# Performance work log

Measured on AMD Instinct MI355X. Metric: run time of the kernel, lower is better.

The kernel has to match this reference:

```python
import jax, jax.numpy as jnp
import numpy as np

FREQ_BANDS = 10
LN_EPS = 1e-5


def nerf_positional_encoding(x, L=FREQ_BANDS):
    # x: (..., 3) -> (..., 3*2*L). Per-frequency [sin(2^i x), cos(2^i x)].
    freqs = 2.0 ** jnp.arange(L, dtype=x.dtype)            # (L,)
    xb = x[..., None, :] * freqs[:, None]                  # (..., L, 3)
    enc = jnp.concatenate([jnp.sin(xb), jnp.cos(xb)], -1)  # (..., L, 6)
    return enc.reshape(x.shape[:-1] + (L * 6,))


def farthest_point_sampling(xyz, npoint):
    # xyz: (B, N, 3) -> (B, npoint) int32. Deterministic start at index 0
    # (torch version uses a random start; start choice is arbitrary for FPS).
    B, N, _ = xyz.shape
    binds = jnp.arange(B)

    def step(carry, _):
        dist, far = carry
        c = xyz[binds, far]                                # (B, 3)
        d = jnp.sum((xyz - c[:, None, :]) ** 2, axis=-1)   # (B, N)
        dist = jnp.minimum(dist, d)
        nxt = jnp.argmax(dist, axis=-1).astype(jnp.int32)
        return (dist, nxt), far

    init = (jnp.full((B, N), 1e10, xyz.dtype), jnp.zeros((B,), jnp.int32))
    _, idx = jax.lax.scan(step, init, None, length=npoint)
    return jnp.swapaxes(idx, 0, 1)                         # (B, npoint)


def _layernorm(x, g, b):
    m = jnp.mean(x, axis=-1, keepdims=True)
    v = jnp.var(x, axis=-1, keepdims=True)
    return (x - m) * jax.lax.rsqrt(v + LN_EPS) * g + b


def setup_inputs() -> dict:
    key = jax.random.key(0)
    ks = jax.random.split(key, 8)
    B, N, C = 8, 16384, 64
    d_in = C + 3 * 2 * FREQ_BANDS                          # 124
    dims = [d_in, 128, 128, 256]

    def lin(k, din, dout):
        return jax.random.normal(k, (din, dout), jnp.float32) / np.sqrt(din)

    return {
        "xyz": jax.random.normal(ks[0], (B, N, 3), jnp.float32),
        "features": jax.random.normal(ks[1], (B, N, C), jnp.float32),
        "W1": lin(ks[2], dims[0], dims[1]), "b1": jnp.zeros((dims[1],), jnp.float32),
        "g1": jnp.ones((dims[1],), jnp.float32), "be1": jnp.zeros((dims[1],), jnp.float32),
        "W2": lin(ks[3], dims[1], dims[2]), "b2": jnp.zeros((dims[2],), jnp.float32),
        "g2": jnp.ones((dims[2],), jnp.float32), "be2": jnp.zeros((dims[2],), jnp.float32),
        "W3": lin(ks[4], dims[2], dims[3]), "b3": jnp.zeros((dims[3],), jnp.float32),
        "npoint": 2048,
        "nsample": 32,
    }


def reference(xyz, features, W1, b1, g1, be1, W2, b2, g2, be2, W3, b3, npoint, nsample):
    # FPS centroids
    fps_idx = farthest_point_sampling(xyz, npoint)                 # (B, S)
    new_xyz = jnp.take_along_axis(xyz, fps_idx[..., None], axis=1) # (B, S, 3)

    # KNN: squared distances preserve topk ordering of cdist
    d2 = jnp.sum((new_xyz[:, :, None, :] - xyz[:, None, :, :]) ** 2, axis=-1)  # (B,S,N)
    _, knn_idx = jax.lax.top_k(-d2, nsample)                        # (B, S, k)

    gather = jax.vmap(lambda pts, idx: pts[idx])                    # (N,D),(S,k)->(S,k,D)
    grouped_xyz = gather(xyz, knn_idx)                              # (B, S, k, 3)
    rel_pos = grouped_xyz - new_xyz[:, :, None, :]
    rel_enc = nerf_positional_encoding(rel_pos)                     # (B, S, k, 60)

    grouped_feat = gather(features, knn_idx)                        # (B, S, k, C)
    h = jnp.concatenate([grouped_feat, rel_enc], axis=-1)           # (B, S, k, C+60)

    h = jax.nn.relu(_layernorm(h @ W1 + b1, g1, be1))
    h = jax.nn.relu(_layernorm(h @ W2 + b2, g2, be2))
    h = h @ W3 + b3                                                 # (B, S, k, 256)
    new_features = jnp.max(h, axis=2)                               # (B, S, 256)
    return new_xyz, new_features
```

## Files before the change

### kernel.cpp

```cpp
#include <hip/hip_runtime.h>
#include <cstdint>
#include <cstddef>

#define BATCH   8
#define NPTS    16384
#define CFEAT   64
#define NPOINT  2048
#define NSAMPLE 32
#define DIN     124
#define D1      128
#define D2      128
#define D3      256
#define LN_EPS  1e-5f

#define NFPS      8
#define NBLOCKS   256
#define KNN_ITEMS 128
#define MLP_ITEMS 2048
#define TOT_ITEMS (KNN_ITEMS + MLP_ITEMS)

#define SB_BYTES   19872
#define SMEM_BYTES (8 * SB_BYTES)

#define CTL_QHEAD   0
#define CTL_PROG    1024
#define CTL_KCNT    4096
#define CTL_KFLAG   16384
#define CTL_BYTES   32768

#define PTS16(F) F(0) F(1) F(2) F(3) F(4) F(5) F(6) F(7) \
                 F(8) F(9) F(10) F(11) F(12) F(13) F(14) F(15)

__attribute__((amdgpu_waves_per_eu(4, 4)))
__global__ __launch_bounds__(1024) void fused_kernel(
    const float* __restrict__ xyz, const float* __restrict__ features,
    const float* __restrict__ W1, const float* __restrict__ b1,
    const float* __restrict__ g1, const float* __restrict__ be1,
    const float* __restrict__ W2, const float* __restrict__ b2,
    const float* __restrict__ g2, const float* __restrict__ be2,
    const float* __restrict__ W3, const float* __restrict__ b3,
    int* __restrict__ knn_idx, unsigned char* __restrict__ ctl,
    float* __restrict__ new_xyz, float* __restrict__ out)
{
  __shared__ __align__(16) unsigned char smem[SMEM_BYTES];
  __shared__ unsigned s_item;
  const int t = threadIdx.x;

  unsigned* qhead = (unsigned*)(ctl + CTL_QHEAD);
#define PROG_AT(b)  ((int*)(ctl + CTL_PROG + (b) * 256))
#define KCNT_AT(k)  ((unsigned*)(ctl + CTL_KCNT + (k) * 64))
#define KFLAG_AT(k) ((unsigned*)(ctl + CTL_KFLAG + (k) * 64))

  if (blockIdx.x < NFPS) {
    const int b = blockIdx.x;
    const float* X = xyz + (size_t)b * NPTS * 3;

    float4 (*s_mind4)[1024] = reinterpret_cast<float4(*)[1024]>(smem);
    float* wvv = (float*)(smem + 65536);
    unsigned long long* s_packed = (unsigned long long*)(smem + 65600);
    float* cbuf = (float*)(smem + 65616);

#define DECLP(i) float px##i, py##i, pz##i;
    PTS16(DECLP)
#undef DECLP
#define LOADP(i) { int j = t + (i << 10);  \
    px##i = X[3 * j + 0];                  \
    py##i = X[3 * j + 1];                  \
    pz##i = X[3 * j + 2]; }
    PTS16(LOADP)
#undef LOADP
    s_mind4[0][t] = make_float4(1e10f, 1e10f, 1e10f, 1e10f);
    s_mind4[1][t] = make_float4(1e10f, 1e10f, 1e10f, 1e10f);
    s_mind4[2][t] = make_float4(1e10f, 1e10f, 1e10f, 1e10f);
    s_mind4[3][t] = make_float4(1e10f, 1e10f, 1e10f, 1e10f);

    if (t == 0) { cbuf[0] = X[0]; cbuf[1] = X[1]; cbuf[2] = X[2]; *s_packed = 0ull; }
    __syncthreads();

    for (int s = 0; s < NPOINT; ++s) {
      const float cx = cbuf[0], cy = cbuf[1], cz = cbuf[2];
      if (t == 0) {
        float* o = new_xyz + ((size_t)b * NPOINT + s) * 3;
        o[0] = cx; o[1] = cy; o[2] = cz;
        *s_packed = 0ull;
        if (((s + 1) & 15) == 0) {
          __builtin_amdgcn_fence(__ATOMIC_RELEASE, "agent");
          __hip_atomic_store(PROG_AT(b), s + 1, __ATOMIC_RELAXED,
                             __HIP_MEMORY_SCOPE_AGENT);
        }
      }
      if (s == NPOINT - 1) break;

      asm volatile("" : "+v"(px0), "+v"(px1), "+v"(px2), "+v"(px3),
                        "+v"(px4), "+v"(px5), "+v"(px6), "+v"(px7),
                        "+v"(px8), "+v"(px9), "+v"(px10), "+v"(px11),
                        "+v"(px12), "+v"(px13), "+v"(px14), "+v"(px15));
      asm volatile("" : "+v"(py0), "+v"(py1), "+v"(py2), "+v"(py3),
                        "+v"(py4), "+v"(py5), "+v"(py6), "+v"(py7),
                        "+v"(py8), "+v"(py9), "+v"(py10), "+v"(py11),
                        "+v"(py12), "+v"(py13), "+v"(py14), "+v"(py15));
      asm volatile("" : "+v"(pz0), "+v"(pz1), "+v"(pz2), "+v"(pz3),
                        "+v"(pz4), "+v"(pz5), "+v"(pz6), "+v"(pz7),
                        "+v"(pz8), "+v"(pz9), "+v"(pz10), "+v"(pz11),
                        "+v"(pz12), "+v"(pz13), "+v"(pz14), "+v"(pz15));

      float mybest = -1.0f;
#define DIST(i) ({                                                       \
    float dx_ = __fsub_rn(px##i, cx);                                    \
    float dy_ = __fsub_rn(py##i, cy);                                    \
    float dz_ = __fsub_rn(pz##i, cz);                                    \
    __fadd_rn(__fadd_rn(__fmul_rn(dx_, dx_), __fmul_rn(dy_, dy_)),       \
              __fmul_rn(dz_, dz_)); })
#define PACKSTEP(p, i0, i1, i2, i3) {                                    \
    float4 dv = s_mind4[p][t];                                           \
    dv.x = fminf(dv.x, DIST(i0));                                        \
    dv.y = fminf(dv.y, DIST(i1));                                        \
    dv.z = fminf(dv.z, DIST(i2));                                        \
    dv.w = fminf(dv.w, DIST(i3));                                        \
    s_mind4[p][t] = dv;                                                  \
    mybest = fmaxf(mybest, fmaxf(fmaxf(dv.x, dv.y), fmaxf(dv.z, dv.w))); }
      PACKSTEP(0, 0, 1, 2, 3)
      PACKSTEP(1, 4, 5, 6, 7)
      PACKSTEP(2, 8, 9, 10, 11)
      PACKSTEP(3, 12, 13, 14, 15)
#undef PACKSTEP
#undef DIST

      float wmax = mybest;
#pragma unroll
      for (int off = 32; off >= 1; off >>= 1)
        wmax = fmaxf(wmax, __shfl_xor(wmax, off));
      if ((t & 63) == 0) wvv[t >> 6] = wmax;
      __syncthreads();

      float4 v0 = *(const float4*)&wvv[0];
      float4 v1 = *(const float4*)&wvv[4];
      float4 v2 = *(const float4*)&wvv[8];
      float4 v3 = *(const float4*)&wvv[12];
      float g = fmaxf(
          fmaxf(fmaxf(fmaxf(v0.x, v0.y), fmaxf(v0.z, v0.w)),
                fmaxf(fmaxf(v1.x, v1.y), fmaxf(v1.z, v1.w))),
          fmaxf(fmaxf(fmaxf(v2.x, v2.y), fmaxf(v2.z, v2.w)),
                fmaxf(fmaxf(v3.x, v3.y), fmaxf(v3.z, v3.w))));

      if (mybest == g) {
        int kk = 16;
#pragma unroll
        for (int p = 3; p >= 0; --p) {
          float4 dv = s_mind4[p][t];
          if (dv.w == g) kk = 4 * p + 3;
          if (dv.z == g) kk = 4 * p + 2;
          if (dv.y == g) kk = 4 * p + 1;
          if (dv.x == g) kk = 4 * p + 0;
        }
        unsigned idx = (unsigned)(t + (kk << 10));
        unsigned long long pk =
            ((unsigned long long)__float_as_uint(g) << 32) | (unsigned)(~idx);
        atomicMax(s_packed, pk);
      }
      __syncthreads();

      unsigned long long gp = *s_packed;
      int widx = (int)(~(unsigned)(gp & 0xffffffffull)) & 0x3fff;
      if (t == (widx & 1023)) {
        int c = widx >> 10;
#define OWNK(i) if (c == i) { cbuf[0] = px##i; cbuf[1] = py##i; cbuf[2] = pz##i; }
        PTS16(OWNK)
#undef OWNK
      }
      __syncthreads();
    }
    return;
  }

  for (;;) {
    __syncthreads();
    if (t == 0)
      s_item = __hip_atomic_fetch_add(qhead, 1u, __ATOMIC_RELAXED,
                                      __HIP_MEMORY_SCOPE_AGENT);
    __syncthreads();
    unsigned item = s_item;
    if (item >= TOT_ITEMS) return;

    if (item < KNN_ITEMS) {
      const int k = (int)item;
      const int b = k >> 4;
      const int chunk = k & 15;
      const int lane = t & 63;
      const int wid  = t >> 6;
      const int gidbase = b * NPOINT + chunk * 128 + wid * 8;
      const int need = chunk * 128 + wid * 8 + 8;
      const float* X = xyz + (size_t)b * NPTS * 3;

      if (lane == 0) {
        while (__hip_atomic_load(PROG_AT(b), __ATOMIC_RELAXED,
                                 __HIP_MEMORY_SCOPE_AGENT) < need)
          __builtin_amdgcn_s_sleep(64);
      }
      __builtin_amdgcn_fence(__ATOMIC_ACQUIRE, "agent");

      float cx[8], cy[8], cz[8];
#pragma unroll
      for (int c = 0; c < 8; ++c) {
        const float* p = new_xyz + (size_t)(gidbase + c) * 3;
        cx[c] = p[0]; cy[c] = p[1]; cz[c] = p[2];
      }
      float qd[8]; int qi[8]; float T[8];
#pragma unroll
      for (int c = 0; c < 8; ++c) { qd[c] = 3.4e38f; qi[c] = 0; T[c] = 3.4e38f; }

      for (int base = 0; base < NPTS; base += 64) {
        const int j = base + lane;
        const float x = X[3 * j + 0];
        const float y = X[3 * j + 1];
        const float z = X[3 * j + 2];
#pragma unroll
        for (int c = 0; c < 8; ++c) {
          float dx = __fsub_rn(x, cx[c]);
          float dy = __fsub_rn(y, cy[c]);
          float dz = __fsub_rn(z, cz[c]);
          float v  = __fadd_rn(__fadd_rn(__fmul_rn(dx, dx), __fmul_rn(dy, dy)),
                               __fmul_rn(dz, dz));
          unsigned long long m = __ballot(v < T[c]);
          while (m) {
            int bit = __ffsll(m) - 1;
            m &= m - 1;
            float vb = __shfl(v, bit);
            if (vb < T[c]) {
              int   jb = base + bit;
              float du = __shfl_up(qd[c], 1);
              int   iu = __shfl_up(qi[c], 1);
              bool c2 = (lane > 0) && (vb < du);
              bool c1 = vb < qd[c];
              qd[c] = c2 ? du : (c1 ? vb : qd[c]);
              qi[c] = c2 ? iu : (c1 ? jb : qi[c]);
              T[c] = __shfl(qd[c], 31);
            }
          }
        }
      }
#pragma unroll
      for (int c = 0; c < 8; ++c) {
        if (lane < 32) knn_idx[(size_t)(gidbase + c) * NSAMPLE + lane] = qi[c];
      }
      __builtin_amdgcn_fence(__ATOMIC_RELEASE, "agent");
      if (lane == 0) {
        unsigned d = __hip_atomic_fetch_add(KCNT_AT(k), 1u, __ATOMIC_ACQ_REL,
                                            __HIP_MEMORY_SCOPE_AGENT);
        if (d == 15u)
          __hip_atomic_store(KFLAG_AT(k), 1u, __ATOMIC_RELEASE,
                             __HIP_MEMORY_SCOPE_AGENT);
      }
    } else {
      const int m = (int)(item - KNN_ITEMS);
      const int gbase = m << 3;
      const int b = gbase / NPOINT;
      const int sb = t >> 7;
      const int t127 = t & 127;
      const int g = gbase + sb;

      if (t == 0) {
        while (__hip_atomic_load(KFLAG_AT(m >> 4), __ATOMIC_RELAXED,
                                 __HIP_MEMORY_SCOPE_AGENT) == 0u)
          __builtin_amdgcn_s_sleep(64);
      }
      __syncthreads();
      __builtin_amdgcn_fence(__ATOMIC_ACQUIRE, "agent");

      unsigned char* base_ = smem + sb * SB_BYTES;
      float* bufT = (float*)base_;
      float (*red)[4][2] = (float(*)[4][2])(base_ + 18432);
      float (*lnp)[2]    = (float(*)[2])(base_ + 19456);
      int*   ki          = (int*)(base_ + 19712);
      float* cen         = (float*)(base_ + 19840);

      if (t127 < 32) ki[t127] = knn_idx[(size_t)g * NSAMPLE + t127];
      if (t127 < 3)  cen[t127] = new_xyz[(size_t)g * 3 + t127];
      __syncthreads();

      {
        int r = t127 & 31, cs = (t127 >> 5) << 4;
        const float* frow = features + ((size_t)b * NPTS + ki[r]) * CFEAT + cs;
#pragma unroll
        for (int u = 0; u < 4; ++u) {
          float4 f = *(const float4*)(frow + 4 * u);
          bufT[(cs + 4 * u + 0) * 36 + r] = f.x;
          bufT[(cs + 4 * u + 1) * 36 + r] = f.y;
          bufT[(cs + 4 * u + 2) * 36 + r] = f.z;
          bufT[(cs + 4 * u + 3) * 36 + r] = f.w;
        }
      }
      if (t127 < 32) {
        const float* p = xyz + ((size_t)b * NPTS + ki[t127]) * 3;
        float rx = p[0] - cen[0];
        float ry = p[1] - cen[1];
        float rz = p[2] - cen[2];
#pragma unroll
        for (int l = 0; l < 10; ++l) {
          float sc = (float)(1 << l);
          float ax = rx * sc, ay = ry * sc, az = rz * sc;
          int bbi = (64 + l * 6) * 36 + t127;
          bufT[bbi + 0 * 36] = __sinf(ax);
          bufT[bbi + 1 * 36] = __sinf(ay);
          bufT[bbi + 2 * 36] = __sinf(az);
          bufT[bbi + 3 * 36] = __cosf(ax);
          bufT[bbi + 4 * 36] = __cosf(ay);
          bufT[bbi + 5 * 36] = __cosf(az);
        }
      }
      __syncthreads();

      float acc[32];
      {
        float bias = b1[t127];
#pragma unroll
        for (int r = 0; r < 32; ++r) acc[r] = bias;
        for (int i = 0; i < DIN; ++i) {
          float w = W1[i * D1 + t127];
          const float* hr = &bufT[i * 36];
#pragma unroll
          for (int r = 0; r < 32; ++r) acc[r] = fmaf(hr[r], w, acc[r]);
        }
      }
      {
        __syncthreads();
#pragma unroll
        for (int r = 0; r < 32; ++r) bufT[t127 * 36 + r] = acc[r];
        __syncthreads();
        {
          int r = t127 & 31, seg = t127 >> 5;
          float s = 0.f, ss = 0.f;
#pragma unroll
          for (int u = 0; u < 32; ++u) {
            float v = bufT[(seg * 32 + u) * 36 + r];
            s += v; ss = fmaf(v, v, ss);
          }
          red[r][seg][0] = s; red[r][seg][1] = ss;
        }
        __syncthreads();
        if (t127 < 32) {
          float s  = red[t127][0][0] + red[t127][1][0] + red[t127][2][0] + red[t127][3][0];
          float ss = red[t127][0][1] + red[t127][1][1] + red[t127][2][1] + red[t127][3][1];
          float mm = s * (1.0f / D1);
          float var = ss * (1.0f / D1) - mm * mm;
          lnp[t127][0] = mm;
          lnp[t127][1] = rsqrtf(var + LN_EPS);
        }
        __syncthreads();
        float gg = g1[t127], bb = be1[t127];
#pragma unroll
        for (int r = 0; r < 32; ++r) {
          float v = (acc[r] - lnp[r][0]) * lnp[r][1];
          v = fmaf(v, gg, bb);
          bufT[t127 * 36 + r] = fmaxf(v, 0.f);
        }
        __syncthreads();
      }
      {
        float bias = b2[t127];
#pragma unroll
        for (int r = 0; r < 32; ++r) acc[r] = bias;
        for (int i = 0; i < D1; ++i) {
          float w = W2[i * D2 + t127];
          const float* hr = &bufT[i * 36];
#pragma unroll
          for (int r = 0; r < 32; ++r) acc[r] = fmaf(hr[r], w, acc[r]);
        }
      }
      {
        __syncthreads();
#pragma unroll
        for (int r = 0; r < 32; ++r) bufT[t127 * 36 + r] = acc[r];
        __syncthreads();
        {
          int r = t127 & 31, seg = t127 >> 5;
          float s = 0.f, ss = 0.f;
#pragma unroll
          for (int u = 0; u < 32; ++u) {
            float v = bufT[(seg * 32 + u) * 36 + r];
            s += v; ss = fmaf(v, v, ss);
          }
          red[r][seg][0] = s; red[r][seg][1] = ss;
        }
        __syncthreads();
        if (t127 < 32) {
          float s  = red[t127][0][0] + red[t127][1][0] + red[t127][2][0] + red[t127][3][0];
          float ss = red[t127][0][1] + red[t127][1][1] + red[t127][2][1] + red[t127][3][1];
          float mm = s * (1.0f / D2);
          float var = ss * (1.0f / D2) - mm * mm;
          lnp[t127][0] = mm;
          lnp[t127][1] = rsqrtf(var + LN_EPS);
        }
        __syncthreads();
        float gg = g2[t127], bb = be2[t127];
#pragma unroll
        for (int r = 0; r < 32; ++r) {
          float v = (acc[r] - lnp[r][0]) * lnp[r][1];
          v = fmaf(v, gg, bb);
          bufT[t127 * 36 + r] = fmaxf(v, 0.f);
        }
        __syncthreads();
      }
      float* of = out + (size_t)g * D3;
#pragma unroll 1
      for (int half = 0; half < 2; ++half) {
        int col = t127 + (half << 7);
        float a[32];
        float bias = b3[col];
#pragma unroll
        for (int r = 0; r < 32; ++r) a[r] = bias;
        for (int i = 0; i < D2; ++i) {
          float w = W3[i * D3 + col];
          const float* hr = &bufT[i * 36];
#pragma unroll
          for (int r = 0; r < 32; ++r) a[r] = fmaf(hr[r], w, a[r]);
        }
        float m0 = a[0];
#pragma unroll
        for (int r = 1; r < 32; ++r) m0 = fmaxf(m0, a[r]);
        of[col] = m0;
      }
      __syncthreads();
    }
  }
#undef PROG_AT
#undef KCNT_AT
#undef KFLAG_AT
}

extern "C" void kernel_launch(void* const* d_in, const int* in_sizes, int n_in,
                              void* d_out, int out_size, void* d_ws, size_t ws_size,
                              hipStream_t stream) {
  const float* xyz      = (const float*)d_in[0];
  const float* features = (const float*)d_in[1];
  const float* W1  = (const float*)d_in[2];
  const float* b1  = (const float*)d_in[3];
  const float* g1  = (const float*)d_in[4];
  const float* be1 = (const float*)d_in[5];
  const float* W2  = (const float*)d_in[6];
  const float* b2  = (const float*)d_in[7];
  const float* g2  = (const float*)d_in[8];
  const float* be2 = (const float*)d_in[9];
  const float* W3  = (const float*)d_in[10];
  const float* b3  = (const float*)d_in[11];

  float* new_xyz  = (float*)d_out;
  float* new_feat = (float*)d_out + (size_t)BATCH * NPOINT * 3;

  int* knn_idx = (int*)d_ws;
  unsigned char* ctl = (unsigned char*)d_ws +
                       (size_t)BATCH * NPOINT * NSAMPLE * 4;

  hipMemsetAsync(ctl, 0, CTL_BYTES, stream);
  fused_kernel<<<dim3(NBLOCKS), dim3(1024), 0, stream>>>(
      xyz, features, W1, b1, g1, be1, W2, b2, g2, be2, W3, b3,
      knn_idx, ctl, new_xyz, new_feat);
}
```

Baseline: 5.087 ms.

## Spatially sort FPS points into Morton grid cells and skip waves by bounding-box bound

Before the FPS loop, each batch's points are bucketed into an 8x8x8 Morton-ordered grid through global scratch arrays and reloaded so every wavefront holds a spatially compact set. Each wave keeps its bounding box and skips the distance update when the box's lower-bound distance to the new centroid cannot beat the wave's current maximum min-distance. Ties in the argmax are broken by original index to keep the output identical. This adds a one-time sort with atomics and a global round trip, plus extra LDS and register pressure, in exchange for skipping most distance work in later iterations. The barriers and reductions per step are unchanged, and some leftover no-op code blocks remain.

Measured after the change: 4.834 ms. 1.05x faster.

```diff
diff --git a/kernel.cpp b/kernel.cpp
--- a/kernel.cpp
+++ b/kernel.cpp
@@ -30,6 +30,11 @@
 
 #define PTS16(F) F(0) F(1) F(2) F(3) F(4) F(5) F(6) F(7) \
                  F(8) F(9) F(10) F(11) F(12) F(13) F(14) F(15)
+
+__device__ float          g_sx[BATCH][NPTS];
+__device__ float          g_sy[BATCH][NPTS];
+__device__ float          g_sz[BATCH][NPTS];
+__device__ unsigned short g_so[BATCH][NPTS];
 
 __attribute__((amdgpu_waves_per_eu(4, 4)))
 __global__ __launch_bounds__(1024) void fused_kernel(
@@ -56,9 +61,15 @@
     const float* X = xyz + (size_t)b * NPTS * 3;
 
     float4 (*s_mind4)[1024] = reinterpret_cast<float4(*)[1024]>(smem);
-    float* wvv = (float*)(smem + 65536);
-    unsigned long long* s_packed = (unsigned long long*)(smem + 65600);
-    float* cbuf = (float*)(smem + 65616);
+    unsigned short* s_oidx  = (unsigned short*)(smem + 65536);
+    float* wvv              = (float*)(smem + 98304);
+    unsigned long long* s_packed = (unsigned long long*)(smem + 98368);
+    float* cbuf             = (float*)(smem + 98432);
+    float (*wbb)[6]         = (float(*)[6])(smem + 98496);
+    float* gpar             = (float*)(smem + 98944);
+    unsigned* cstart        = (unsigned*)(smem + 99008);
+    unsigned* ccur          = (unsigned*)(smem + 101120);
+    float (*redbuf)[6]      = (float(*)[6])(smem + 103168);
 
 #define DECLP(i) float px##i, py##i, pz##i;
     PTS16(DECLP)
@@ -69,16 +80,137 @@
     pz##i = X[3 * j + 2]; }
     PTS16(LOADP)
 #undef LOADP
+
+    {
+      float mnx = px0, mxx = px0, mny = py0, mxy = py0, mnz = pz0, mxz = pz0;
+#define BB(i) { mnx = fminf(mnx, px##i); mxx = fmaxf(mxx, px##i);  \
+                mny = fminf(mny, py##i); mxy = fmaxf(mxy, py##i);  \
+                mnz = fminf(mnz, pz##i); mxz = fmaxf(mxz, pz##i); }
+      PTS16(BB)
+#undef BB
+#pragma unroll
+      for (int off = 32; off >= 1; off >>= 1) {
+        mnx = fminf(mnx, __shfl_xor(mnx, off)); mxx = fmaxf(mxx, __shfl_xor(mxx, off));
+        mny = fminf(mny, __shfl_xor(mny, off)); mxy = fmaxf(mxy, __shfl_xor(mxy, off));
+        mnz = fminf(mnz, __shfl_xor(mnz, off)); mxz = fmaxf(mxz, __shfl_xor(mxz, off));
+      }
+      if ((t & 63) == 0) {
+        int w = t >> 6;
+        redbuf[w][0] = mnx; redbuf[w][1] = mxx; redbuf[w][2] = mny;
+        redbuf[w][3] = mxy; redbuf[w][4] = mnz; redbuf[w][5] = mxz;
+      }
+      if (t < 513) cstart[t] = 0;
+      __syncthreads();
+      if (t == 0) {
+        float a0 = redbuf[0][0], a1 = redbuf[0][1], a2 = redbuf[0][2];
+        float a3 = redbuf[0][3], a4 = redbuf[0][4], a5 = redbuf[0][5];
+        for (int w = 1; w < 16; ++w) {
+          a0 = fminf(a0, redbuf[w][0]); a1 = fmaxf(a1, redbuf[w][1]);
+          a2 = fminf(a2, redbuf[w][2]); a3 = fmaxf(a3, redbuf[w][3]);
+          a4 = fminf(a4, redbuf[w][4]); a5 = fmaxf(a5, redbuf[w][5]);
+        }
+        float rx = a1 - a0, ry = a3 - a2, rz = a5 - a4;
+        gpar[0] = a0; gpar[1] = a2; gpar[2] = a4;
+        gpar[3] = (rx > 1e-20f) ? 8.0f / rx : 0.f;
+        gpar[4] = (ry > 1e-20f) ? 8.0f / ry : 0.f;
+        gpar[5] = (rz > 1e-20f) ? 8.0f / rz : 0.f;
+        cbuf[0] = X[0]; cbuf[1] = X[1]; cbuf[2] = X[2];
+        *s_packed = 0ull;
+      }
+      __syncthreads();
+    }
+
+#define CELLM(x, y, z) ({                                              \
+    int ix_ = (int)((x - gpar[0]) * gpar[3]);                          \
+    int iy_ = (int)((y - gpar[1]) * gpar[4]);                          \
+    int iz_ = (int)((z - gpar[2]) * gpar[5]);                          \
+    ix_ = ix_ < 0 ? 0 : (ix_ > 7 ? 7 : ix_);                           \
+    iy_ = iy_ < 0 ? 0 : (iy_ > 7 ? 7 : iy_);                           \
+    iz_ = iz_ < 0 ? 0 : (iz_ > 7 ? 7 : iz_);                           \
+    (((ix_ & 1) | ((ix_ & 2) << 2) | ((ix_ & 4) << 4))                 \
+     | (((iy_ & 1) | ((iy_ & 2) << 2) | ((iy_ & 4) << 4)) << 1)        \
+     | (((iz_ & 1) | ((iz_ & 2) << 2) | ((iz_ & 4) << 4)) << 2)); })
+
+#define CIDK(i) { int m_ = CELLM(px##i, py##i, pz##i); \
+    atomicAdd(&cstart[m_ + 1], 1u); }
+    PTS16(CIDK)
+#undef CIDK
+    __syncthreads();
+
+    if (t < 64) {
+      unsigned v[8], p[8];
+      unsigned run = 0;
+#pragma unroll
+      for (int j = 0; j < 8; ++j) { v[j] = cstart[t * 8 + 1 + j]; run += v[j]; p[j] = run; }
+      unsigned tot = run;
+#pragma unroll
+      for (int off = 1; off < 64; off <<= 1) {
+        unsigned u = __shfl_up(run, off);
+        if ((t & 63) >= off) run += u;
+      }
+      unsigned excl = run - tot;
+      if (t == 0) cstart[0] = 0;
+#pragma unroll
+      for (int j = 0; j < 8; ++j) cstart[t * 8 + 1 + j] = excl + p[j];
+    }
+    __syncthreads();
+    if (t < 512) ccur[t] = cstart[t];
+    __syncthreads();
+
+#define SCATK(i) { int j = t + (i << 10);                              \
+    int m_ = CELLM(px##i, py##i, pz##i);                               \
+    unsigned dst = atomicAdd(&ccur[m_], 1u);                           \
+    g_sx[b][dst] = px##i; g_sy[b][dst] = py##i; g_sz[b][dst] = pz##i;  \
+    g_so[b][dst] = (unsigned short)j; }
+    PTS16(SCATK)
+#undef SCATK
+#undef CELLM
+    __syncthreads();
+
+    float tlx = 1e30f, thx = -1e30f, tly = 1e30f, thy = -1e30f,
+          tlz = 1e30f, thz = -1e30f;
+#define RELK(i) { int p_ = (t << 4) + i;                               \
+    px##i = g_sx[b][p_]; py##i = g_sy[b][p_]; pz##i = g_sz[b][p_];     \
+    s_oidx[(i << 10) + t] = g_so[b][p_];                               \
+    tlx = fminf(tlx, px##i); thx = fmaxf(thx, px##i);                  \
+    tly = fminf(tly, py##i); thy = fmaxf(thy, py##i);                  \
+    tlz = fminf(tlz, pz##i); thz = fmaxf(thz, pz##i); }
+    PTS16(RELK)
+#undef RELK
     s_mind4[0][t] = make_float4(1e10f, 1e10f, 1e10f, 1e10f);
     s_mind4[1][t] = make_float4(1e10f, 1e10f, 1e10f, 1e10f);
     s_mind4[2][t] = make_float4(1e10f, 1e10f, 1e10f, 1e10f);
     s_mind4[3][t] = make_float4(1e10f, 1e10f, 1e10f, 1e10f);
 
-    if (t == 0) { cbuf[0] = X[0]; cbuf[1] = X[1]; cbuf[2] = X[2]; *s_packed = 0ull; }
+#pragma unroll
+    for (int off = 32; off >= 1; off >>= 1) {
+      tlx = fminf(tlx, __shfl_xor(tlx, off)); thx = fmaxf(thx, __shfl_xor(thx, off));
+      tly = fminf(tly, __shfl_xor(tly, off)); thy = fmaxf(thy, __shfl_xor(thy, off));
+      tlz = fminf(tlz, __shfl_xor(tlz, off)); thz = fmaxf(thz, __shfl_xor(thz, off));
+    }
+    if ((t & 63) == 0) {
+      int w = t >> 6;
+      wbb[w][0] = tlx; wbb[w][1] = thx; wbb[w][2] = tly;
+      wbb[w][3] = thy; wbb[w][4] = tlz; wbb[w][5] = thz;
+    }
+
+    float mybest = -1.0f;
+    float wvmax  = 1e10f;
+    int   far    = 0;
     __syncthreads();
 
     for (int s = 0; s < NPOINT; ++s) {
       const float cx = cbuf[0], cy = cbuf[1], cz = cbuf[2];
+      if (t == 0) {
+        fps_idx_write:;
+        ((int*)0 == (int*)0);
+      }
+      if (t == 0) {
+        int* fi = (int*)knn_idx;
+        (void)fi;
+      }
+      if (t == 0) {
+      }
       if (t == 0) {
         float* o = new_xyz + ((size_t)b * NPOINT + s) * 3;
         o[0] = cx; o[1] = cy; o[2] = cz;
@@ -104,7 +236,17 @@
                         "+v"(pz8), "+v"(pz9), "+v"(pz10), "+v"(pz11),
                         "+v"(pz12), "+v"(pz13), "+v"(pz14), "+v"(pz15));
 
-      float mybest = -1.0f;
+      {
+        const int w = t >> 6;
+        float lox = wbb[w][0], hix = wbb[w][1];
+        float loy = wbb[w][2], hiy = wbb[w][3];
+        float loz = wbb[w][4], hiz = wbb[w][5];
+        float ddx = fmaxf(fmaxf(lox - cx, cx - hix), 0.f);
+        float ddy = fmaxf(fmaxf(loy - cy, cy - hiy), 0.f);
+        float ddz = fmaxf(fmaxf(loz - cz, cz - hiz), 0.f);
+        float dlb2 = ddx * ddx + ddy * ddy + ddz * ddz;
+        if (dlb2 < wvmax * 1.0001f) {
+          mybest = -1.0f;
 #define DIST(i) ({                                                       \
     float dx_ = __fsub_rn(px##i, cx);                                    \
     float dy_ = __fsub_rn(py##i, cy);                                    \
@@ -119,18 +261,20 @@
     dv.w = fminf(dv.w, DIST(i3));                                        \
     s_mind4[p][t] = dv;                                                  \
     mybest = fmaxf(mybest, fmaxf(fmaxf(dv.x, dv.y), fmaxf(dv.z, dv.w))); }
-      PACKSTEP(0, 0, 1, 2, 3)
-      PACKSTEP(1, 4, 5, 6, 7)
-      PACKSTEP(2, 8, 9, 10, 11)
-      PACKSTEP(3, 12, 13, 14, 15)
+          PACKSTEP(0, 0, 1, 2, 3)
+          PACKSTEP(1, 4, 5, 6, 7)
+          PACKSTEP(2, 8, 9, 10, 11)
+          PACKSTEP(3, 12, 13, 14, 15)
 #undef PACKSTEP
 #undef DIST
-
-      float wmax = mybest;
-#pragma unroll
-      for (int off = 32; off >= 1; off >>= 1)
-        wmax = fmaxf(wmax, __shfl_xor(wmax, off));
-      if ((t & 63) == 0) wvv[t >> 6] = wmax;
+          float wmax = mybest;
+#pragma unroll
+          for (int off = 32; off >= 1; off >>= 1)
+            wmax = fmaxf(wmax, __shfl_xor(wmax, off));
+          wvmax = wmax;
+          if ((t & 63) == 0) wvv[w] = wmax;
+        }
+      }
       __syncthreads();
 
       float4 v0 = *(const float4*)&wvv[0];
@@ -144,26 +288,32 @@
                 fmaxf(fmaxf(v3.x, v3.y), fmaxf(v3.z, v3.w))));
 
       if (mybest == g) {
-        int kk = 16;
-#pragma unroll
-        for (int p = 3; p >= 0; --p) {
+        unsigned bo = 0xFFFFu; int bk = 0;
+#pragma unroll
+        for (int p = 0; p < 4; ++p) {
           float4 dv = s_mind4[p][t];
-          if (dv.w == g) kk = 4 * p + 3;
-          if (dv.z == g) kk = 4 * p + 2;
-          if (dv.y == g) kk = 4 * p + 1;
-          if (dv.x == g) kk = 4 * p + 0;
-        }
-        unsigned idx = (unsigned)(t + (kk << 10));
+          { unsigned o = s_oidx[((4 * p + 0) << 10) + t];
+            if (dv.x == g && o < bo) { bo = o; bk = 4 * p + 0; } }
+          { unsigned o = s_oidx[((4 * p + 1) << 10) + t];
+            if (dv.y == g && o < bo) { bo = o; bk = 4 * p + 1; } }
+          { unsigned o = s_oidx[((4 * p + 2) << 10) + t];
+            if (dv.z == g && o < bo) { bo = o; bk = 4 * p + 2; } }
+          { unsigned o = s_oidx[((4 * p + 3) << 10) + t];
+            if (dv.w == g && o < bo) { bo = o; bk = 4 * p + 3; } }
+        }
+        unsigned payload = ((~bo & 0x3FFFu) << 14) | (unsigned)((t << 4) | bk);
         unsigned long long pk =
-            ((unsigned long long)__float_as_uint(g) << 32) | (unsigned)(~idx);
+            ((unsigned long long)__float_as_uint(g) << 32) | payload;
         atomicMax(s_packed, pk);
       }
       __syncthreads();
 
       unsigned long long gp = *s_packed;
-      int widx = (int)(~(unsigned)(gp & 0xffffffffull)) & 0x3fff;
-      if (t == (widx & 1023)) {
-        int c = widx >> 10;
+      unsigned pl = (unsigned)(gp & 0xffffffffull);
+      far = (int)((~(pl >> 14)) & 0x3FFFu);
+      int spos = (int)(pl & 0x3FFFu);
+      if (t == (spos >> 4)) {
+        int c = spos & 15;
 #define OWNK(i) if (c == i) { cbuf[0] = px##i; cbuf[1] = py##i; cbuf[2] = pz##i; }
         PTS16(OWNK)
 #undef OWNK
```
